# Optimization experiments

Measured on AMD Instinct MI355X. Metric: run time of the kernel, lower is better.

The kernel has to match this reference:

```python
import jax, jax.numpy as jnp
import numpy as np

B = 65536
NC = 64          # coarse samples
NF = 128         # fine samples
NEAR, FAR = 2.0, 6.0


def setup_inputs() -> dict:
    key = jax.random.key(0)
    k1, k2, k3, k4, k5, k6 = jax.random.split(key, 6)
    ray_origin = jax.random.normal(k1, (B, 3), dtype=jnp.float32)
    ray_direction = jax.random.normal(k2, (B, 3), dtype=jnp.float32)
    # stratified linspace depths, as in the coarse branch of _sample_points_on_ray
    step = (FAR - NEAR) / (NC - 1)
    coarse_depth_values = jnp.broadcast_to(
        NEAR + jnp.arange(NC, dtype=jnp.float32) * step, (B, NC)
    )
    coarse_weights = jax.random.uniform(k3, (B, NC), dtype=jnp.float32)
    u = jax.random.uniform(k4, (B, NF), dtype=jnp.float32)
    raw_density = jax.random.uniform(k5, (B, NC + NF, 1), dtype=jnp.float32)
    raw_color = jax.random.uniform(k6, (B, NC + NF, 3), dtype=jnp.float32)
    return {
        "ray_origin": ray_origin,
        "ray_direction": ray_direction,
        "coarse_depth_values": coarse_depth_values,
        "coarse_weights": coarse_weights,
        "u": u,
        "raw_density": raw_density,
        "raw_color": raw_color,
    }


def _sample_pdf(bins, weights, u):
    """Inverse-CDF sampling. bins: [B, M+1], weights: [B, M], u: [B, N]."""
    M = weights.shape[1]
    weights = weights + 1e-5
    pdf = weights / jnp.sum(weights, axis=-1, keepdims=True)
    cdf = jnp.cumsum(pdf, axis=-1)                     # [B, M]
    cdf = jnp.concatenate([jnp.zeros_like(cdf[:, :1]), cdf], axis=-1)  # [B, M+1]
    # torch loop `above_inds += (u >= cdf[:, i])` for i in [0, M) ==
    # searchsorted(cdf[:, :M], u, side='right')
    above = jax.vmap(lambda c, uu: jnp.searchsorted(c, uu, side="right"))(
        cdf[:, :M], u
    )                                                  # [B, N], values in [1, M]
    below = jnp.clip(above - 1, 0, None)
    cdf_b = jnp.take_along_axis(cdf, below, axis=-1)
    cdf_a = jnp.take_along_axis(cdf, above, axis=-1)
    bins_b = jnp.take_along_axis(bins, below, axis=-1)
    bins_a = jnp.take_along_axis(bins, above, axis=-1)
    denom = cdf_a - cdf_b
    denom = jnp.where(denom < 1e-5, jnp.ones_like(denom), denom)
    t = (u - cdf_b) / denom
    return bins_b + t * (bins_a - bins_b)


def _composite(raw_density, raw_color, depth_values):
    # distances between consecutive samples, last one = 1e10
    dists = depth_values[..., 1:] - depth_values[..., :-1]
    dists = jnp.concatenate(
        [dists, jnp.full_like(dists[:, :1], 1e10)], axis=-1
    )
    alpha = 1.0 - jnp.exp(-raw_density[..., 0] * dists)          # [B, S]
    T = jnp.cumprod(1.0 - alpha + 1e-10, axis=-1)[:, :-1]
    T = jnp.concatenate([jnp.ones_like(T[:, :1]), T], axis=-1)
    weights = T * alpha                                           # [B, S]
    depth = jnp.sum(weights * depth_values, axis=-1, keepdims=True)
    color = jnp.sum(weights[..., None] * raw_color, axis=-2)      # [B, 3]
    return depth, color, weights


def reference(ray_origin, ray_direction, coarse_depth_values, coarse_weights,
              u, raw_density, raw_color):
    # fine branch of _sample_points_on_ray
    mids = 0.5 * (coarse_depth_values[..., 1:] + coarse_depth_values[..., :-1])
    w = coarse_weights[:, 1:-1]
    fine_depths = _sample_pdf(mids, w, u)                         # [B, NF]
    depth_values = jnp.sort(
        jnp.concatenate([coarse_depth_values, fine_depths], axis=-1), axis=-1
    )                                                             # [B, NC+NF]
    points_on_ray = (
        ray_origin[:, None, :]
        + ray_direction[:, None, :] * depth_values[..., None]
    )                                                             # [B, S, 3]
    depth, color_map, weights = _composite(raw_density, raw_color, depth_values)
    # forward of RenderRay returns the color map; points kept live via dummy use
    del points_on_ray, depth, weights
    return color_map
```

## Files before the change

kernel.cpp:

```cpp
#include <hip/hip_runtime.h>

#define NC 64
#define NF 128
#define NT 192
#define B_TOTAL 65536
#define RPB 4

#define NEAR_F 2.0f
#define STEP_F (4.0f / 63.0f)
#define INV_STEP (63.0f / 4.0f)

template<int CTRL, int RM>
__device__ __forceinline__ float updpp_f(float oldv, float v) {
    return __int_as_float(__builtin_amdgcn_update_dpp(
        __float_as_int(oldv), __float_as_int(v), CTRL, RM, 0xf, false));
}
template<int CTRL, int RM>
__device__ __forceinline__ int updpp_i(int oldv, int v) {
    return __builtin_amdgcn_update_dpp(oldv, v, CTRL, RM, 0xf, false);
}

__device__ __forceinline__ float wave_iscan_add_f(float v) {
    v += updpp_f<0x111, 0xf>(0.0f, v);
    v += updpp_f<0x112, 0xf>(0.0f, v);
    v += updpp_f<0x114, 0xf>(0.0f, v);
    v += updpp_f<0x118, 0xf>(0.0f, v);
    v += updpp_f<0x142, 0xa>(0.0f, v);
    v += updpp_f<0x143, 0xc>(0.0f, v);
    return v;
}
__device__ __forceinline__ float wave_iscan_mul_f(float v) {
    v *= updpp_f<0x111, 0xf>(1.0f, v);
    v *= updpp_f<0x112, 0xf>(1.0f, v);
    v *= updpp_f<0x114, 0xf>(1.0f, v);
    v *= updpp_f<0x118, 0xf>(1.0f, v);
    v *= updpp_f<0x142, 0xa>(1.0f, v);
    v *= updpp_f<0x143, 0xc>(1.0f, v);
    return v;
}
__device__ __forceinline__ int wave_iscan_add_i(int v) {
    v += updpp_i<0x111, 0xf>(0, v);
    v += updpp_i<0x112, 0xf>(0, v);
    v += updpp_i<0x114, 0xf>(0, v);
    v += updpp_i<0x118, 0xf>(0, v);
    v += updpp_i<0x142, 0xa>(0, v);
    v += updpp_i<0x143, 0xc>(0, v);
    return v;
}

__device__ __forceinline__ float rlane_f(float v, int l) {
    return __int_as_float(__builtin_amdgcn_readlane(__float_as_int(v), l));
}

__device__ __forceinline__ void wave_fence() {
    __builtin_amdgcn_wave_barrier();
    __asm__ volatile("" ::: "memory");
}

__global__ __launch_bounds__(256) void render_ray_kernel(
    const float* __restrict__ cw,
    const float* __restrict__ u_in,
    const float* __restrict__ dens,
    const float* __restrict__ col,
    float* __restrict__ out)
{
    const int wave = threadIdx.x >> 6;
    const int lane = threadIdx.x & 63;
    const int ray  = blockIdx.x * RPB + wave;

    __shared__ float s_cdf [RPB][64];
    __shared__ float s_m   [RPB][200];
    __shared__ int   s_hist[RPB][64];

    const float wraw = cw[(size_t)ray * NC + lane];
    float x = u_in[(size_t)ray * NF + lane];
    float y = u_in[(size_t)ray * NF + 64 + lane];

    const int i0 = 3 * lane;
    const float* __restrict__ dp = dens + (size_t)ray * NT + i0;
    const float dv0 = dp[0], dv1 = dp[1], dv2 = dp[2];
    const float* __restrict__ cp = col + ((size_t)ray * NT + (size_t)i0) * 3;
    float cc[9];
    #pragma unroll
    for (int q = 0; q < 9; ++q) cc[q] = cp[q];

    const float wv = (lane >= 1 && lane <= 62) ? (wraw + 1e-5f) : 0.0f;
    const float sc = wave_iscan_add_f(wv);
    const float total = rlane_f(sc, 63);
    const float cdfv = __fdividef(sc, total);
    s_cdf[wave][lane]  = cdfv;
    s_hist[wave][lane] = 0;

    const float c31 = rlane_f(cdfv, 31);
    const float c15 = rlane_f(cdfv, 15), c47 = rlane_f(cdfv, 47);
    const float c7  = rlane_f(cdfv, 7),  c23 = rlane_f(cdfv, 23);
    const float c39 = rlane_f(cdfv, 39), c55 = rlane_f(cdfv, 55);
    wave_fence();

    #pragma unroll
    for (int k = 2; k <= 128; k <<= 1) {
        #pragma unroll
        for (int j = k >> 1; j > 0; j >>= 1) {
            if (j == 64) {
                const float mn = fminf(x, y);
                const float mx = fmaxf(x, y);
                x = mn; y = mx;
            } else {
                const bool up = (lane & j) != 0;
                const bool dx = (lane & k) != 0;
                const bool dy = ((lane + 64) & k) != 0;
                const float px = __shfl_xor(x, j);
                const float py = __shfl_xor(y, j);
                const bool cx = x < px;
                const bool cy = y < py;
                x = ((cx != up) != dx) ? x : px;
                y = ((cy != up) != dy) ? y : py;
            }
        }
    }

    const float* __restrict__ cdfp = s_cdf[wave];
    auto sample = [&](float u, int& g) -> float {
        int l = (c31 <= u) ? 32 : 0;
        const float p16 = (l == 0) ? c15 : c47;
        if (p16 <= u) l += 16;
        const float pa = ((l & 16) == 0) ? c7  : c23;
        const float pb = ((l & 16) == 0) ? c39 : c55;
        const float p8 = ((l & 32) == 0) ? pa : pb;
        if (p8 <= u) l += 8;
        if (cdfp[l + 3] <= u) l += 4;
        if (cdfp[l + 1] <= u) l += 2;
        if (cdfp[l]     <= u) l += 1;
        l = min(l, 62);
        const int below = l - 1;
        const float cb = cdfp[below];
        const float ca = cdfp[l];
        float denom = ca - cb;
        if (denom < 1e-5f) denom = 1.0f;
        const float t = __fdividef(u - cb, denom);
        const float f = NEAR_F + ((float)below + 0.5f + t) * STEP_F;
        int gi = (int)floorf((f - NEAR_F) * INV_STEP) + 1;
        g = min(max(gi, 1), 63);
        return f;
    };

    int gx, gy;
    const float fx = sample(x, gx);
    const float fy = sample(y, gy);

    s_m[wave][lane + gx]      = fx;
    s_m[wave][lane + 64 + gy] = fy;
    atomicAdd(&s_hist[wave][gx], 1);
    atomicAdd(&s_hist[wave][gy], 1);
    wave_fence();

    const int hsum = wave_iscan_add_i(s_hist[wave][lane]);
    s_m[wave][lane + hsum] = NEAR_F + (float)lane * STEP_F;
    wave_fence();

    const float* __restrict__ mp = s_m[wave];
    const float m0 = mp[i0], m1 = mp[i0 + 1], m2 = mp[i0 + 2];
    const float m3 = mp[i0 + 3];
    const float d0 = m1 - m0;
    const float d1 = m2 - m1;
    const float d2 = (lane == 63) ? 1e10f : (m3 - m2);

    const float a0 = 1.0f - __expf(-dv0 * d0);
    const float a1 = 1.0f - __expf(-dv1 * d1);
    const float a2 = 1.0f - __expf(-dv2 * d2);
    const float f0 = 1.0f - a0 + 1e-10f;
    const float f1 = 1.0f - a1 + 1e-10f;
    const float f2 = 1.0f - a2 + 1e-10f;

    const float prod  = f0 * f1 * f2;
    const float scanp = wave_iscan_mul_f(prod);
    const float T0 = __fdividef(scanp, prod);
    const float T1 = T0 * f0;
    const float T2 = T1 * f1;

    const float w0 = T0 * (1.0f - f0 + 1e-10f);
    const float w1 = T1 * (1.0f - f1 + 1e-10f);
    const float w2 = T2 * (1.0f - f2 + 1e-10f);

    float ax = w0 * cc[0] + w1 * cc[3] + w2 * cc[6];
    float ay = w0 * cc[1] + w1 * cc[4] + w2 * cc[7];
    float az = w0 * cc[2] + w1 * cc[5] + w2 * cc[8];

    ax = wave_iscan_add_f(ax);
    ay = wave_iscan_add_f(ay);
    az = wave_iscan_add_f(az);
    if (lane == 63) {
        out[(size_t)ray * 3 + 0] = ax;
        out[(size_t)ray * 3 + 1] = ay;
        out[(size_t)ray * 3 + 2] = az;
    }
}

extern "C" void kernel_launch(void* const* d_in, const int* in_sizes, int n_in,
                              void* d_out, int out_size, void* d_ws, size_t ws_size,
                              hipStream_t stream) {
    const float* cwts = (const float*)d_in[3];
    const float* u    = (const float*)d_in[4];
    const float* dens = (const float*)d_in[5];
    const float* col  = (const float*)d_in[6];
    float* out = (float*)d_out;

    dim3 grid(B_TOTAL / RPB);
    dim3 block(256);
    hipLaunchKernelGGL(render_ray_kernel, grid, block, 0, stream,
                       cwts, u, dens, col, out);
}
```

Baseline: 288.1 us.

## Process two rays per wavefront to interleave independent work and raise ILP

Each wave now handles two rays instead of one, with every stage (loads, CDF scan, bitonic sort, sampling, histogram merge, compositing scans) interleaved across both rays. The aim is to hide shuffle, DPP and LDS latency with independent instruction streams and to keep more loads in flight per wave. Grid size halves and shared memory per block doubles. The launch bound now requests 8 blocks per SM, which with the doubled register footprint may cap registers and risk spills.

Result: no change. 293.7 us (+1.9%).

```diff
diff --git a/kernel.cpp b/kernel.cpp
--- a/kernel.cpp
+++ b/kernel.cpp
@@ -4,7 +4,9 @@
 #define NF 128
 #define NT 192
 #define B_TOTAL 65536
-#define RPB 4
+#define RPW 2
+#define WPB 4
+#define RPB (RPW * WPB)
 
 #define NEAR_F 2.0f
 #define STEP_F (4.0f / 63.0f)
@@ -57,7 +59,7 @@
     __asm__ volatile("" ::: "memory");
 }
 
-__global__ __launch_bounds__(256) void render_ray_kernel(
+__global__ __launch_bounds__(256, 8) void render_ray_kernel(
     const float* __restrict__ cw,
     const float* __restrict__ u_in,
     const float* __restrict__ dens,
@@ -66,35 +68,44 @@
 {
     const int wave = threadIdx.x >> 6;
     const int lane = threadIdx.x & 63;
-    const int ray  = blockIdx.x * RPB + wave;
+    const int ray0 = blockIdx.x * RPB + wave * RPW;
+    const int wr   = wave * RPW;
 
     __shared__ float s_cdf [RPB][64];
     __shared__ float s_m   [RPB][200];
     __shared__ int   s_hist[RPB][64];
 
-    const float wraw = cw[(size_t)ray * NC + lane];
-    float x = u_in[(size_t)ray * NF + lane];
-    float y = u_in[(size_t)ray * NF + 64 + lane];
-
     const int i0 = 3 * lane;
-    const float* __restrict__ dp = dens + (size_t)ray * NT + i0;
-    const float dv0 = dp[0], dv1 = dp[1], dv2 = dp[2];
-    const float* __restrict__ cp = col + ((size_t)ray * NT + (size_t)i0) * 3;
-    float cc[9];
-    #pragma unroll
-    for (int q = 0; q < 9; ++q) cc[q] = cp[q];
-
-    const float wv = (lane >= 1 && lane <= 62) ? (wraw + 1e-5f) : 0.0f;
-    const float sc = wave_iscan_add_f(wv);
-    const float total = rlane_f(sc, 63);
-    const float cdfv = __fdividef(sc, total);
-    s_cdf[wave][lane]  = cdfv;
-    s_hist[wave][lane] = 0;
-
-    const float c31 = rlane_f(cdfv, 31);
-    const float c15 = rlane_f(cdfv, 15), c47 = rlane_f(cdfv, 47);
-    const float c7  = rlane_f(cdfv, 7),  c23 = rlane_f(cdfv, 23);
-    const float c39 = rlane_f(cdfv, 39), c55 = rlane_f(cdfv, 55);
+
+    float x[RPW], y[RPW];
+    float dv0[RPW], dv1[RPW], dv2[RPW];
+    float cc[RPW][9];
+    float c31[RPW], c15[RPW], c47[RPW];
+    float c7[RPW], c23[RPW], c39[RPW], c55[RPW];
+
+    #pragma unroll
+    for (int r = 0; r < RPW; ++r) {
+        const size_t ray = (size_t)(ray0 + r);
+        const float wraw = cw[ray * NC + lane];
+        x[r] = u_in[ray * NF + lane];
+        y[r] = u_in[ray * NF + 64 + lane];
+        const float* __restrict__ dp = dens + ray * NT + i0;
+        dv0[r] = dp[0]; dv1[r] = dp[1]; dv2[r] = dp[2];
+        const float* __restrict__ cp = col + (ray * NT + (size_t)i0) * 3;
+        #pragma unroll
+        for (int q = 0; q < 9; ++q) cc[r][q] = cp[q];
+
+        const float wv = (lane >= 1 && lane <= 62) ? (wraw + 1e-5f) : 0.0f;
+        const float sc = wave_iscan_add_f(wv);
+        const float total = rlane_f(sc, 63);
+        const float cdfv = __fdividef(sc, total);
+        s_cdf[wr + r][lane]  = cdfv;
+        s_hist[wr + r][lane] = 0;
+        c31[r] = rlane_f(cdfv, 31);
+        c15[r] = rlane_f(cdfv, 15); c47[r] = rlane_f(cdfv, 47);
+        c7 [r] = rlane_f(cdfv, 7);  c23[r] = rlane_f(cdfv, 23);
+        c39[r] = rlane_f(cdfv, 39); c55[r] = rlane_f(cdfv, 55);
+    }
     wave_fence();
 
     #pragma unroll
@@ -102,32 +113,43 @@
         #pragma unroll
         for (int j = k >> 1; j > 0; j >>= 1) {
             if (j == 64) {
-                const float mn = fminf(x, y);
-                const float mx = fmaxf(x, y);
-                x = mn; y = mx;
+                #pragma unroll
+                for (int r = 0; r < RPW; ++r) {
+                    const float mn = fminf(x[r], y[r]);
+                    const float mx = fmaxf(x[r], y[r]);
+                    x[r] = mn; y[r] = mx;
+                }
             } else {
                 const bool up = (lane & j) != 0;
                 const bool dx = (lane & k) != 0;
                 const bool dy = ((lane + 64) & k) != 0;
-                const float px = __shfl_xor(x, j);
-                const float py = __shfl_xor(y, j);
-                const bool cx = x < px;
-                const bool cy = y < py;
-                x = ((cx != up) != dx) ? x : px;
-                y = ((cy != up) != dy) ? y : py;
+                float px[RPW], py[RPW];
+                #pragma unroll
+                for (int r = 0; r < RPW; ++r) {
+                    px[r] = __shfl_xor(x[r], j);
+                    py[r] = __shfl_xor(y[r], j);
+                }
+                #pragma unroll
+                for (int r = 0; r < RPW; ++r) {
+                    const bool cx = x[r] < px[r];
+                    const bool cy = y[r] < py[r];
+                    x[r] = ((cx != up) != dx) ? x[r] : px[r];
+                    y[r] = ((cy != up) != dy) ? y[r] : py[r];
+                }
             }
         }
     }
 
-    const float* __restrict__ cdfp = s_cdf[wave];
-    auto sample = [&](float u, int& g) -> float {
-        int l = (c31 <= u) ? 32 : 0;
-        const float p16 = (l == 0) ? c15 : c47;
-        if (p16 <= u) l += 16;
-        const float pa = ((l & 16) == 0) ? c7  : c23;
-        const float pb = ((l & 16) == 0) ? c39 : c55;
-        const float p8 = ((l & 32) == 0) ? pa : pb;
-        if (p8 <= u) l += 8;
+    auto sample = [&](const float* __restrict__ cdfp, float u,
+                      float p31, float p15, float p47, float p7f,
+                      float p23, float p39, float p55, int& g) -> float {
+        int l = (p31 <= u) ? 32 : 0;
+        const float q16 = (l == 0) ? p15 : p47;
+        if (q16 <= u) l += 16;
+        const float pa = ((l & 16) == 0) ? p7f : p23;
+        const float pb = ((l & 16) == 0) ? p39 : p55;
+        const float q8 = ((l & 32) == 0) ? pa : pb;
+        if (q8 <= u) l += 8;
         if (cdfp[l + 3] <= u) l += 4;
         if (cdfp[l + 1] <= u) l += 2;
         if (cdfp[l]     <= u) l += 1;
@@ -144,55 +166,72 @@
         return f;
     };
 
-    int gx, gy;
-    const float fx = sample(x, gx);
-    const float fy = sample(y, gy);
-
-    s_m[wave][lane + gx]      = fx;
-    s_m[wave][lane + 64 + gy] = fy;
-    atomicAdd(&s_hist[wave][gx], 1);
-    atomicAdd(&s_hist[wave][gy], 1);
+    #pragma unroll
+    for (int r = 0; r < RPW; ++r) {
+        int gx, gy;
+        const float fx = sample(s_cdf[wr + r], x[r], c31[r], c15[r], c47[r],
+                                c7[r], c23[r], c39[r], c55[r], gx);
+        const float fy = sample(s_cdf[wr + r], y[r], c31[r], c15[r], c47[r],
+                                c7[r], c23[r], c39[r], c55[r], gy);
+        s_m[wr + r][lane + gx]      = fx;
+        s_m[wr + r][lane + 64 + gy] = fy;
+        atomicAdd(&s_hist[wr + r][gx], 1);
+        atomicAdd(&s_hist[wr + r][gy], 1);
+    }
     wave_fence();
 
-    const int hsum = wave_iscan_add_i(s_hist[wave][lane]);
-    s_m[wave][lane + hsum] = NEAR_F + (float)lane * STEP_F;
+    #pragma unroll
+    for (int r = 0; r < RPW; ++r) {
+        const int hsum = wave_iscan_add_i(s_hist[wr + r][lane]);
+        s_m[wr + r][lane + hsum] = NEAR_F + (float)lane * STEP_F;
+    }
     wave_fence();
 
-    const float* __restrict__ mp = s_m[wave];
-    const float m0 = mp[i0], m1 = mp[i0 + 1], m2 = mp[i0 + 2];
-    const float m3 = mp[i0 + 3];
-    const float d0 = m1 - m0;
-    const float d1 = m2 - m1;
-    const float d2 = (lane == 63) ? 1e10f : (m3 - m2);
-
-    const float a0 = 1.0f - __expf(-dv0 * d0);
-    const float a1 = 1.0f - __expf(-dv1 * d1);
-    const float a2 = 1.0f - __expf(-dv2 * d2);
-    const float f0 = 1.0f - a0 + 1e-10f;
-    const float f1 = 1.0f - a1 + 1e-10f;
-    const float f2 = 1.0f - a2 + 1e-10f;
-
-    const float prod  = f0 * f1 * f2;
-    const float scanp = wave_iscan_mul_f(prod);
-    const float T0 = __fdividef(scanp, prod);
-    const float T1 = T0 * f0;
-    const float T2 = T1 * f1;
-
-    const float w0 = T0 * (1.0f - f0 + 1e-10f);
-    const float w1 = T1 * (1.0f - f1 + 1e-10f);
-    const float w2 = T2 * (1.0f - f2 + 1e-10f);
-
-    float ax = w0 * cc[0] + w1 * cc[3] + w2 * cc[6];
-    float ay = w0 * cc[1] + w1 * cc[4] + w2 * cc[7];
-    float az = w0 * cc[2] + w1 * cc[5] + w2 * cc[8];
-
-    ax = wave_iscan_add_f(ax);
-    ay = wave_iscan_add_f(ay);
-    az = wave_iscan_add_f(az);
+    float ax[RPW], ay[RPW], az[RPW];
+    #pragma unroll
+    for (int r = 0; r < RPW; ++r) {
+        const float* __restrict__ mp = s_m[wr + r];
+        const float m0 = mp[i0], m1 = mp[i0 + 1], m2 = mp[i0 + 2];
+        const float m3 = mp[i0 + 3];
+        const float d0 = m1 - m0;
+        const float d1 = m2 - m1;
+        const float d2 = (lane == 63) ? 1e10f : (m3 - m2);
+
+        const float a0 = 1.0f - __expf(-dv0[r] * d0);
+        const float a1 = 1.0f - __expf(-dv1[r] * d1);
+        const float a2 = 1.0f - __expf(-dv2[r] * d2);
+        const float f0 = 1.0f - a0 + 1e-10f;
+        const float f1 = 1.0f - a1 + 1e-10f;
+        const float f2 = 1.0f - a2 + 1e-10f;
+
+        const float prod  = f0 * f1 * f2;
+        const float scanp = wave_iscan_mul_f(prod);
+        const float T0 = __fdividef(scanp, prod);
+        const float T1 = T0 * f0;
+        const float T2 = T1 * f1;
+
+        const float w0 = T0 * (1.0f - f0 + 1e-10f);
+        const float w1 = T1 * (1.0f - f1 + 1e-10f);
+        const float w2 = T2 * (1.0f - f2 + 1e-10f);
+
+        ax[r] = w0 * cc[r][0] + w1 * cc[r][3] + w2 * cc[r][6];
+        ay[r] = w0 * cc[r][1] + w1 * cc[r][4] + w2 * cc[r][7];
+        az[r] = w0 * cc[r][2] + w1 * cc[r][5] + w2 * cc[r][8];
+    }
+
+    #pragma unroll
+    for (int r = 0; r < RPW; ++r) {
+        ax[r] = wave_iscan_add_f(ax[r]);
+        ay[r] = wave_iscan_add_f(ay[r]);
+        az[r] = wave_iscan_add_f(az[r]);
+    }
     if (lane == 63) {
-        out[(size_t)ray * 3 + 0] = ax;
-        out[(size_t)ray * 3 + 1] = ay;
-        out[(size_t)ray * 3 + 2] = az;
+        #pragma unroll
+        for (int r = 0; r < RPW; ++r) {
+            out[(size_t)(ray0 + r) * 3 + 0] = ax[r];
+            out[(size_t)(ray0 + r) * 3 + 1] = ay[r];
+            out[(size_t)(ray0 + r) * 3 + 2] = az[r];
+        }
     }
 }
 
```
